# Kernel optimization log

Measured on AMD Instinct MI355X. Metric: run time of the kernel, lower is better.

The kernel has to match this reference:

```python
import jax, jax.numpy as jnp
import numpy as np

N = 100000      # nodes
E = 1600000     # edges (avg degree 16)
F_IN = 128
F_HID = 128
LN_EPS = 1e-5


def setup_inputs() -> dict:
    key = jax.random.key(0)
    ks = jax.random.split(key, 4)
    x = jax.random.normal(ks[0], (N, F_IN), dtype=jnp.float32)
    edge_index = jax.random.randint(ks[1], (2, E), 0, N, dtype=jnp.int32)
    W1 = jax.random.normal(ks[2], (F_IN, F_HID), dtype=jnp.float32) * 0.05
    W2 = jax.random.normal(ks[3], (F_HID, F_HID), dtype=jnp.float32) * 0.05
    return {
        "x": x,
        "edge_index": edge_index,
        "W1": W1, "b1": jnp.zeros((F_HID,), jnp.float32),
        "W2": W2, "b2": jnp.zeros((F_HID,), jnp.float32),
        "g1": jnp.ones((F_HID,), jnp.float32), "be1": jnp.zeros((F_HID,), jnp.float32),
        "g2": jnp.ones((F_HID,), jnp.float32), "be2": jnp.zeros((F_HID,), jnp.float32),
    }


def layer_norm(x, gamma, beta):
    mu = jnp.mean(x, axis=-1, keepdims=True)
    var = jnp.mean(jnp.square(x - mu), axis=-1, keepdims=True)
    return (x - mu) * jax.lax.rsqrt(var + LN_EPS) * gamma + beta


def gcn_conv(x, src, dst, W, b):
    """PyG GCNConv: linear transform, add self-loops, symmetric-normalized scatter-add."""
    n = x.shape[0]
    loop = jnp.arange(n, dtype=src.dtype)
    s = jnp.concatenate([src, loop])   # [E+N] sources (incl. self-loops)
    d = jnp.concatenate([dst, loop])   # [E+N] destinations
    deg = jax.ops.segment_sum(jnp.ones(s.shape[0], x.dtype), d, num_segments=n)
    dinv = jnp.where(deg > 0, jax.lax.rsqrt(deg), 0.0)
    norm = dinv[s] * dinv[d]           # [E+N] edge normalization
    h = x @ W                          # [N, F_hid] transform BEFORE propagate (PyG order)
    msg = h[s] * norm[:, None]         # [E+N, F_hid] gathered, normalized messages
    out = jax.ops.segment_sum(msg, d, num_segments=n)
    return out + b


def reference(x, edge_index, W1, b1, W2, b2, g1, be1, g2, be2):
    # GCN_body, layer=2, layer_norm_first=False, use_ln=True, eval mode (dropout=identity)
    src, dst = edge_index[0], edge_index[1]
    h = layer_norm(jax.nn.relu(gcn_conv(x, src, dst, W1, b1)), g1, be1)
    h = layer_norm(jax.nn.relu(gcn_conv(h, src, dst, W2, b2)), g2, be2)
    return h
```

## Files before the change

### kernel.cpp

```cpp
#include <hip/hip_runtime.h>

#define FDIM 128
#define LN_EPS 1e-5f
#define BSH 9
#define EPB 2048

typedef short short8 __attribute__((ext_vector_type(8)));
typedef float f32x4 __attribute__((ext_vector_type(4)));

__device__ __forceinline__ ushort f2bf(float f) {
    uint u = __float_as_uint(f);
    u += 0x7fff + ((u >> 16) & 1);
    return (ushort)(u >> 16);
}
__device__ __forceinline__ float bflo(uint u) { return __uint_as_float(u << 16); }
__device__ __forceinline__ float bfhi(uint u) { return __uint_as_float(u & 0xffff0000u); }


__global__ __launch_bounds__(256) void k_bcount(const int* __restrict__ dst,
                                                uint* __restrict__ mat, int nbk, int E) {
    __shared__ uint cnt[512];
    int t = threadIdx.x;
    for (int i = t; i < nbk; i += 256) cnt[i] = 0;
    __syncthreads();
    int base = blockIdx.x * EPB, end = min(base + EPB, E);
    for (int e = base + t; e < end; e += 256)
        atomicAdd(&cnt[(uint)dst[e] >> BSH], 1u);
    __syncthreads();
    for (int i = t; i < nbk; i += 256) mat[(size_t)blockIdx.x * nbk + i] = cnt[i];
}

__global__ __launch_bounds__(1024) void k_colscan(uint* __restrict__ mat,
                                                  uint* __restrict__ btot, int nbk, int nblk) {
    __shared__ uint s[1024];
    int b = blockIdx.x, t = threadIdx.x;
    uint run = 0;
    for (int base = 0; base < nblk; base += 1024) {
        int i = base + t;
        uint v = (i < nblk) ? mat[(size_t)i * nbk + b] : 0;
        s[t] = v;
        __syncthreads();
        for (int off = 1; off < 1024; off <<= 1) {
            uint u = (t >= off) ? s[t - off] : 0;
            __syncthreads();
            s[t] += u;
            __syncthreads();
        }
        if (i < nblk) mat[(size_t)i * nbk + b] = run + s[t] - v;
        run += s[1023];
        __syncthreads();
    }
    if (t == 0) btot[b] = run;
}

__global__ __launch_bounds__(256) void k_bscatter(const int* __restrict__ src,
                                                  const int* __restrict__ dst,
                                                  const uint* __restrict__ mat,
                                                  const uint* __restrict__ btot,
                                                  uint* __restrict__ ebuf, int nbk, int E) {
    __shared__ uint cur[512];
    __shared__ uint ps[256];
    int t = threadIdx.x;
    uint v = (t < nbk) ? btot[t] : 0;
    ps[t] = v;
    __syncthreads();
    for (int off = 1; off < 256; off <<= 1) {
        uint u = (t >= off) ? ps[t - off] : 0;
        __syncthreads();
        ps[t] += u;
        __syncthreads();
    }
    if (t < nbk) cur[t] = (ps[t] - v) + mat[(size_t)blockIdx.x * nbk + t];
    __syncthreads();
    int base = blockIdx.x * EPB, end = min(base + EPB, E);
    for (int e = base + t; e < end; e += 256) {
        uint d = (uint)dst[e];
        uint off = atomicAdd(&cur[d >> BSH], 1u);
        ebuf[off] = ((d & 511u) << 17) | (uint)src[e];
    }
}

__global__ __launch_bounds__(256) void k_bdeg(const uint* __restrict__ ebuf,
                                              const uint* __restrict__ btot,
                                              int* __restrict__ deg, float* __restrict__ dinv,
                                              uint* __restrict__ padtot, int N, int nbk) {
    __shared__ uint cnt[512];
    __shared__ uint ps[256];
    __shared__ uint begs;
    int b = blockIdx.x, t = threadIdx.x;
    for (int i = t; i < 512; i += 256) cnt[i] = 0;
    uint v = (t < nbk) ? btot[t] : 0;
    ps[t] = v;
    __syncthreads();
    for (int off = 1; off < 256; off <<= 1) {
        uint u = (t >= off) ? ps[t - off] : 0;
        __syncthreads();
        ps[t] += u;
        __syncthreads();
    }
    if (t == b) begs = ps[t] - v;
    __syncthreads();
    uint beg = begs, cn = btot[b];
    for (uint i = t; i < cn; i += 256) atomicAdd(&cnt[ebuf[beg + i] >> 17], 1u);
    __syncthreads();
    int n0 = b << BSH;
    uint loc = 0;
    for (int i = t; i < 512; i += 256) {
        int n = n0 + i;
        if (n < N) {
            uint dg = cnt[i];
            deg[n] = (int)dg;
            dinv[n] = rsqrtf((float)dg + 1.0f);
            loc += (dg + 7u) & ~7u;
        }
    }
    ps[t] = loc;
    __syncthreads();
    for (int off = 128; off >= 1; off >>= 1) {
        if (t < off) ps[t] += ps[t + off];
        __syncthreads();
    }
    if (t == 0) padtot[b] = ps[0];
}

__device__ __forceinline__ void bfill_body(const uint* __restrict__ ebuf,
                                           const uint* __restrict__ btot,
                                           const uint* __restrict__ padtot,
                                           const int* __restrict__ deg,
                                           int* __restrict__ rowptr, int* __restrict__ col,
                                           int N, int nbk, int b) {
    __shared__ uint ps[256];
    __shared__ uint lrp[512];
    __shared__ uint curf[512];
    __shared__ uint sc0, sc1;
    int t = threadIdx.x;
    uint v = (t < nbk) ? btot[t] : 0;
    ps[t] = v;
    __syncthreads();
    for (int off = 1; off < 256; off <<= 1) {
        uint u = (t >= off) ? ps[t - off] : 0;
        __syncthreads();
        ps[t] += u;
        __syncthreads();
    }
    if (t == b) sc0 = ps[t] - v;
    __syncthreads();
    uint w = (t < nbk) ? padtot[t] : 0;
    ps[t] = w;
    __syncthreads();
    for (int off = 1; off < 256; off <<= 1) {
        uint u = (t >= off) ? ps[t - off] : 0;
        __syncthreads();
        ps[t] += u;
        __syncthreads();
    }
    if (t == b) sc1 = ps[t] - w;
    if (b == nbk - 1 && t == nbk - 1) rowptr[N] = (int)ps[t];
    __syncthreads();
    uint beg = sc0, cn = btot[b], base = sc1;
    int n0 = b << BSH;
    int nA = n0 + 2 * t, nB = nA + 1;
    uint dA = (nA < N) ? (uint)deg[nA] : 0;
    uint dB = (nB < N) ? (uint)deg[nB] : 0;
    uint pA = (dA + 7u) & ~7u, pB = (dB + 7u) & ~7u;
    uint pair = pA + pB;
    ps[t] = pair;
    __syncthreads();
    for (int off = 1; off < 256; off <<= 1) {
        uint u = (t >= off) ? ps[t - off] : 0;
        __syncthreads();
        ps[t] += u;
        __syncthreads();
    }
    uint pex = ps[t] - pair;
    uint rA = base + pex, rB = rA + pA;
    lrp[2 * t] = rA; lrp[2 * t + 1] = rB;
    curf[2 * t] = rA; curf[2 * t + 1] = rB;
    if (nA < N) rowptr[nA] = (int)rA;
    if (nB < N) rowptr[nB] = (int)rB;
    if (nA < N) for (uint k = dA; k < pA; ++k) col[rA + k] = N;
    if (nB < N) for (uint k = dB; k < pB; ++k) col[rB + k] = N;
    __syncthreads();
    for (uint i = t; i < cn; i += 256) {
        uint e = ebuf[beg + i];
        uint p = atomicAdd(&curf[e >> 17], 1u);
        col[p] = (int)(e & 0x1FFFFu);
    }
}

__global__ void k_wt2(const float* __restrict__ W1, const float* __restrict__ W2,
                      ushort* __restrict__ WT1, ushort* __restrict__ WT2) {
    int b = blockIdx.x, k = threadIdx.x;
    if (b < 128) WT1[b * 128 + k] = f2bf(W1[k * 128 + b]);
    else         WT2[(b - 128) * 128 + k] = f2bf(W2[k * 128 + (b - 128)]);
}

template <bool F32IN>
__device__ __forceinline__ void gemm_body(char* sXb, char* sWb,
                                          const void* __restrict__ Xin,
                                          const ushort* __restrict__ WT,
                                          const float* __restrict__ dinv,
                                          ushort* __restrict__ H, int N, int bid) {
    int t = threadIdx.x;
    int w = t >> 6, lane = t & 63;
    int cl = lane & 15, kq = lane >> 4;
    int base = bid * 64;

    const short8* Wg = (const short8*)WT;
#pragma unroll
    for (int k = 0; k < 8; ++k) {
        int idx = t + k * 256;
        int c = idx >> 4, ch = idx & 15;
        *(short8*)(sWb + c * 256 + ((ch * 16) ^ ((c & 7) << 4))) = Wg[idx];
    }

    if constexpr (F32IN) {
        const float4* X4 = (const float4*)Xin;
        size_t lim = (size_t)N * 32 - 1;
#pragma unroll
        for (int k = 0; k < 8; ++k) {
            int idx = t + k * 256;
            size_t gi = (size_t)base * 32 + idx;
            float4 v = X4[gi < lim ? gi : lim];
            ushort4 o;
            o.x = f2bf(v.x); o.y = f2bf(v.y); o.z = f2bf(v.z); o.w = f2bf(v.w);
            int row = idx >> 5, b8 = (idx & 31) * 8;
            *(ushort4*)(sXb + row * 256 + (b8 ^ ((row & 7) << 4))) = o;
        }
    } else {
        const short8* X8 = (const short8*)Xin;
        size_t lim = (size_t)N * 16 - 1;
#pragma unroll
        for (int k = 0; k < 4; ++k) {
            int idx = t + k * 256;
            size_t gi = (size_t)base * 16 + idx;
            short8 v = X8[gi < lim ? gi : lim];
            int row = idx >> 4, b16 = (idx & 15) * 16;
            *(short8*)(sXb + row * 256 + (b16 ^ ((row & 7) << 4))) = v;
        }
    }
    __syncthreads();

    int rl = w * 16 + cl;
    short8 b0, b1, b2, b3;
#pragma unroll
    for (int kt = 0; kt < 4; ++kt) {
        short8 v = *(const short8*)(sXb + rl * 256 + ((kt * 64 + kq * 16) ^ ((rl & 7) << 4)));
        if (kt == 0) b0 = v; else if (kt == 1) b1 = v; else if (kt == 2) b2 = v; else b3 = v;
    }

    int r = base + rl;
    bool ok = r < N;
    float di = dinv[min(r, N - 1)];
#pragma unroll
    for (int nt = 0; nt < 8; ++nt) {
        int c = nt * 16 + cl;
        int sw = (c & 7) << 4;
        f32x4 acc = {0.f, 0.f, 0.f, 0.f};
        acc = __builtin_amdgcn_mfma_f32_16x16x32_bf16(
            *(const short8*)(sWb + c * 256 + ((0 * 64 + kq * 16) ^ sw)), b0, acc, 0, 0, 0);
        acc = __builtin_amdgcn_mfma_f32_16x16x32_bf16(
            *(const short8*)(sWb + c * 256 + ((1 * 64 + kq * 16) ^ sw)), b1, acc, 0, 0, 0);
        acc = __builtin_amdgcn_mfma_f32_16x16x32_bf16(
            *(const short8*)(sWb + c * 256 + ((2 * 64 + kq * 16) ^ sw)), b2, acc, 0, 0, 0);
        acc = __builtin_amdgcn_mfma_f32_16x16x32_bf16(
            *(const short8*)(sWb + c * 256 + ((3 * 64 + kq * 16) ^ sw)), b3, acc, 0, 0, 0);
        if (ok) {
            ushort4 o;
            o.x = f2bf(acc[0] * di); o.y = f2bf(acc[1] * di);
            o.z = f2bf(acc[2] * di); o.w = f2bf(acc[3] * di);
            *(ushort4*)(H + (size_t)r * 128 + nt * 16 + kq * 4) = o;
        }
    }
}

template <bool F32IN>
__global__ __launch_bounds__(256) void k_gemm(const void* __restrict__ Xin,
                                              const ushort* __restrict__ WT,
                                              const float* __restrict__ dinv,
                                              ushort* __restrict__ H, int N) {
    __shared__ ushort sX[64 * 128];
    __shared__ ushort sW[128 * 128];
    gemm_body<F32IN>((char*)sX, (char*)sW, Xin, WT, dinv, H, N, blockIdx.x);
}

__global__ __launch_bounds__(256) void k_mega(const void* __restrict__ Xin,
                                              const ushort* __restrict__ WT,
                                              const float* __restrict__ dinv,
                                              ushort* __restrict__ H, int N, int ngemm,
                                              const uint* __restrict__ ebuf,
                                              const uint* __restrict__ btot,
                                              const uint* __restrict__ padtot,
                                              const int* __restrict__ deg,
                                              int* __restrict__ rowptr,
                                              int* __restrict__ col, int nbk) {
    __shared__ ushort sX[64 * 128];
    __shared__ ushort sW[128 * 128];
    if (blockIdx.x < (uint)ngemm) {
        gemm_body<true>((char*)sX, (char*)sW, Xin, WT, dinv, H, N, blockIdx.x);
    } else {
        bfill_body(ebuf, btot, padtot, deg, rowptr, col, N, nbk, blockIdx.x - ngemm);
    }
}

__global__ __launch_bounds__(256) void k_agg(const uint4* __restrict__ H4,
                                             const int* __restrict__ rowptr,
                                             const int* __restrict__ col,
                                             const float* __restrict__ dinv,
                                             const float* __restrict__ bias,
                                             const float* __restrict__ gamma,
                                             const float* __restrict__ beta,
                                             float* __restrict__ outf,
                                             uint4* __restrict__ outb,
                                             int N) {
    int wave = threadIdx.x >> 6;
    int lane = threadIdx.x & 63;
    int q = lane >> 4;
    int l = lane & 15;
    int node = blockIdx.x * 16 + wave * 4 + q;
    bool valid = node < N;
    int nodec = valid ? node : N - 1;

    float di = dinv[nodec];
    uint4 hs = H4[(uint)nodec * 16u + (uint)l];
    float a0 = bflo(hs.x), a1 = bfhi(hs.x), a2 = bflo(hs.y), a3 = bfhi(hs.y);
    float a4 = bflo(hs.z), a5 = bfhi(hs.z), a6 = bflo(hs.w), a7 = bfhi(hs.w);

    int beg = rowptr[nodec];
    int deg8 = rowptr[nodec + 1] - beg;
    const int* cp = col + beg;

    for (int i = 0; i < deg8; i += 8) {
        int s0 = cp[i + 0], s1 = cp[i + 1], s2 = cp[i + 2], s3 = cp[i + 3];
        int s4 = cp[i + 4], s5 = cp[i + 5], s6 = cp[i + 6], s7 = cp[i + 7];
        uint4 u0 = H4[(uint)s0 * 16u + (uint)l];
        uint4 u1 = H4[(uint)s1 * 16u + (uint)l];
        uint4 u2 = H4[(uint)s2 * 16u + (uint)l];
        uint4 u3 = H4[(uint)s3 * 16u + (uint)l];
        uint4 u4 = H4[(uint)s4 * 16u + (uint)l];
        uint4 u5 = H4[(uint)s5 * 16u + (uint)l];
        uint4 u6 = H4[(uint)s6 * 16u + (uint)l];
        uint4 u7 = H4[(uint)s7 * 16u + (uint)l];
        a0 += bflo(u0.x); a1 += bfhi(u0.x); a2 += bflo(u0.y); a3 += bfhi(u0.y);
        a4 += bflo(u0.z); a5 += bfhi(u0.z); a6 += bflo(u0.w); a7 += bfhi(u0.w);
        a0 += bflo(u1.x); a1 += bfhi(u1.x); a2 += bflo(u1.y); a3 += bfhi(u1.y);
        a4 += bflo(u1.z); a5 += bfhi(u1.z); a6 += bflo(u1.w); a7 += bfhi(u1.w);
        a0 += bflo(u2.x); a1 += bfhi(u2.x); a2 += bflo(u2.y); a3 += bfhi(u2.y);
        a4 += bflo(u2.z); a5 += bfhi(u2.z); a6 += bflo(u2.w); a7 += bfhi(u2.w);
        a0 += bflo(u3.x); a1 += bfhi(u3.x); a2 += bflo(u3.y); a3 += bfhi(u3.y);
        a4 += bflo(u3.z); a5 += bfhi(u3.z); a6 += bflo(u3.w); a7 += bfhi(u3.w);
        a0 += bflo(u4.x); a1 += bfhi(u4.x); a2 += bflo(u4.y); a3 += bfhi(u4.y);
        a4 += bflo(u4.z); a5 += bfhi(u4.z); a6 += bflo(u4.w); a7 += bfhi(u4.w);
        a0 += bflo(u5.x); a1 += bfhi(u5.x); a2 += bflo(u5.y); a3 += bfhi(u5.y);
        a4 += bflo(u5.z); a5 += bfhi(u5.z); a6 += bflo(u5.w); a7 += bfhi(u5.w);
        a0 += bflo(u6.x); a1 += bfhi(u6.x); a2 += bflo(u6.y); a3 += bfhi(u6.y);
        a4 += bflo(u6.z); a5 += bfhi(u6.z); a6 += bflo(u6.w); a7 += bfhi(u6.w);
        a0 += bflo(u7.x); a1 += bfhi(u7.x); a2 += bflo(u7.y); a3 += bfhi(u7.y);
        a4 += bflo(u7.z); a5 += bfhi(u7.z); a6 += bflo(u7.w); a7 += bfhi(u7.w);
    }

    float4 bb0 = ((const float4*)bias)[2 * l];
    float4 bb1 = ((const float4*)bias)[2 * l + 1];
    a0 = fmaxf(fmaf(a0, di, bb0.x), 0.f);
    a1 = fmaxf(fmaf(a1, di, bb0.y), 0.f);
    a2 = fmaxf(fmaf(a2, di, bb0.z), 0.f);
    a3 = fmaxf(fmaf(a3, di, bb0.w), 0.f);
    a4 = fmaxf(fmaf(a4, di, bb1.x), 0.f);
    a5 = fmaxf(fmaf(a5, di, bb1.y), 0.f);
    a6 = fmaxf(fmaf(a6, di, bb1.z), 0.f);
    a7 = fmaxf(fmaf(a7, di, bb1.w), 0.f);

    float s1 = ((a0 + a1) + (a2 + a3)) + ((a4 + a5) + (a6 + a7));
    float s2 = ((a0 * a0 + a1 * a1) + (a2 * a2 + a3 * a3)) +
               ((a4 * a4 + a5 * a5) + (a6 * a6 + a7 * a7));
#pragma unroll
    for (int off = 8; off >= 1; off >>= 1) {
        s1 += __shfl_xor(s1, off);
        s2 += __shfl_xor(s2, off);
    }
    float mu = s1 * (1.f / 128.f);
    float var = s2 * (1.f / 128.f) - mu * mu;
    float rs = rsqrtf(var + LN_EPS);

    float4 g0 = ((const float4*)gamma)[2 * l];
    float4 g1 = ((const float4*)gamma)[2 * l + 1];
    float4 e0 = ((const float4*)beta)[2 * l];
    float4 e1 = ((const float4*)beta)[2 * l + 1];
    float o0 = (a0 - mu) * rs * g0.x + e0.x;
    float o1 = (a1 - mu) * rs * g0.y + e0.y;
    float o2 = (a2 - mu) * rs * g0.z + e0.z;
    float o3 = (a3 - mu) * rs * g0.w + e0.w;
    float o4 = (a4 - mu) * rs * g1.x + e1.x;
    float o5 = (a5 - mu) * rs * g1.y + e1.y;
    float o6 = (a6 - mu) * rs * g1.z + e1.z;
    float o7 = (a7 - mu) * rs * g1.w + e1.w;

    if (!valid) return;
    if (outf) {
        ((float4*)outf)[(size_t)node * 32 + 2 * l]     = make_float4(o0, o1, o2, o3);
        ((float4*)outf)[(size_t)node * 32 + 2 * l + 1] = make_float4(o4, o5, o6, o7);
    } else {
        uint4 o;
        o.x = (uint)f2bf(o0) | ((uint)f2bf(o1) << 16);
        o.y = (uint)f2bf(o2) | ((uint)f2bf(o3) << 16);
        o.z = (uint)f2bf(o4) | ((uint)f2bf(o5) << 16);
        o.w = (uint)f2bf(o6) | ((uint)f2bf(o7) << 16);
        outb[(size_t)node * 16 + l] = o;
    }
}

extern "C" void kernel_launch(void* const* d_in, const int* in_sizes, int n_in,
                              void* d_out, int out_size, void* d_ws, size_t ws_size,
                              hipStream_t stream) {
    const float* x  = (const float*)d_in[0];
    const int*   ei = (const int*)d_in[1];
    const float* W1 = (const float*)d_in[2];
    const float* b1 = (const float*)d_in[3];
    const float* W2 = (const float*)d_in[4];
    const float* b2 = (const float*)d_in[5];
    const float* g1 = (const float*)d_in[6];
    const float* be1 = (const float*)d_in[7];
    const float* g2 = (const float*)d_in[8];
    const float* be2 = (const float*)d_in[9];

    int N = in_sizes[0] / FDIM;
    int E = in_sizes[1] / 2;
    const int* srcp = ei;
    const int* dstp = ei + E;
    float* out = (float*)d_out;

    char* w = (char*)d_ws;
    size_t off = 0;
    auto take = [&](size_t bytes) {
        void* p = w + off;
        off = (off + bytes + 255) & ~(size_t)255;
        return p;
    };
    int nbk  = (N + 511) >> BSH;
    int nblk = (E + EPB - 1) / EPB;

    ushort* hb   = (ushort*)take((size_t)(N + 1) * FDIM * sizeof(ushort));
    ushort* WT1  = (ushort*)take(128 * 128 * sizeof(ushort));
    ushort* WT2  = (ushort*)take(128 * 128 * sizeof(ushort));
    uint* mat    = (uint*)take((size_t)nblk * nbk * sizeof(uint));
    uint* btot   = (uint*)take((size_t)nbk * sizeof(uint));
    uint* padtot = (uint*)take((size_t)nbk * sizeof(uint));
    uint* ebuf   = (uint*)take((size_t)E * sizeof(uint));
    int* deg     = (int*)take((size_t)N * sizeof(int));
    int* rowptr  = (int*)take((size_t)(N + 1) * sizeof(int));
    int* colb    = (int*)take((size_t)(E + 7 * (size_t)N + 1024) * sizeof(int));
    float* dinv  = (float*)take((size_t)N * sizeof(float));
    (void)ws_size;

    int ngemm = (N + 63) / 64;

    hipMemsetAsync(hb + (size_t)N * FDIM, 0, FDIM * sizeof(ushort), stream);

    k_wt2<<<256, 128, 0, stream>>>(W1, W2, WT1, WT2);

    k_bcount<<<nblk, 256, 0, stream>>>(dstp, mat, nbk, E);
    k_colscan<<<nbk, 1024, 0, stream>>>(mat, btot, nbk, nblk);
    k_bscatter<<<nblk, 256, 0, stream>>>(srcp, dstp, mat, btot, ebuf, nbk, E);
    k_bdeg<<<nbk, 256, 0, stream>>>(ebuf, btot, deg, dinv, padtot, N, nbk);

    k_mega<<<ngemm + nbk, 256, 0, stream>>>(x, WT1, dinv, hb, N, ngemm,
                                            ebuf, btot, padtot, deg, rowptr, colb, nbk);

    k_agg<<<(N + 15) / 16, 256, 0, stream>>>((const uint4*)hb, rowptr, colb, dinv,
                                             b1, g1, be1, nullptr, (uint4*)d_out, N);
    k_gemm<false><<<ngemm, 256, 0, stream>>>(d_out, WT2, dinv, hb, N);
    k_agg<<<(N + 15) / 16, 256, 0, stream>>>((const uint4*)hb, rowptr, colb, dinv,
                                             b2, g2, be2, out, nullptr, N);
}
```

Measured before the change: 221.7 us.

## Slice hidden features into eight column planes for cache-local aggregation

Stores the transformed features as eight 16-column slices so that each aggregation block gathers from a single 3.2MB slice. The goal is to keep the random neighbour gathers resident in cache. Because each block now sees only part of a row, LayerNorm is split into partial sums per slice, a small stats kernel, and a normalization step. That step is folded into the second GEMM's input load or done by a final apply kernel. It adds two extra kernels and extra traffic for the partial stats and the intermediate bf16 activations, and it reuses the output buffer and the edge-sort scratch as temporaries.

```diff
diff --git a/kernel.cpp b/kernel.cpp
--- a/kernel.cpp
+++ b/kernel.cpp
@@ -15,7 +15,7 @@
 }
 __device__ __forceinline__ float bflo(uint u) { return __uint_as_float(u << 16); }
 __device__ __forceinline__ float bfhi(uint u) { return __uint_as_float(u & 0xffff0000u); }
-
+__device__ __forceinline__ float bfs(short s) { return __uint_as_float(((uint)(ushort)s) << 16); }
 
 __global__ __launch_bounds__(256) void k_bcount(const int* __restrict__ dst,
                                                 uint* __restrict__ mat, int nbk, int E) {
@@ -130,7 +130,6 @@
                                            int* __restrict__ rowptr, int* __restrict__ col,
                                            int N, int nbk, int b) {
     __shared__ uint ps[256];
-    __shared__ uint lrp[512];
     __shared__ uint curf[512];
     __shared__ uint sc0, sc1;
     int t = threadIdx.x;
@@ -174,7 +173,6 @@
     }
     uint pex = ps[t] - pair;
     uint rA = base + pex, rB = rA + pA;
-    lrp[2 * t] = rA; lrp[2 * t + 1] = rB;
     curf[2 * t] = rA; curf[2 * t + 1] = rB;
     if (nA < N) rowptr[nA] = (int)rA;
     if (nB < N) rowptr[nB] = (int)rB;
@@ -189,17 +187,25 @@
 }
 
 __global__ void k_wt2(const float* __restrict__ W1, const float* __restrict__ W2,
-                      ushort* __restrict__ WT1, ushort* __restrict__ WT2) {
+                      ushort* __restrict__ WT1, ushort* __restrict__ WT2,
+                      ushort* __restrict__ H, int N) {
     int b = blockIdx.x, k = threadIdx.x;
-    if (b < 128) WT1[b * 128 + k] = f2bf(W1[k * 128 + b]);
-    else         WT2[(b - 128) * 128 + k] = f2bf(W2[k * 128 + (b - 128)]);
-}
-
-template <bool F32IN>
+    if (b < 128)      WT1[b * 128 + k] = f2bf(W1[k * 128 + b]);
+    else if (b < 256) WT2[(b - 128) * 128 + k] = f2bf(W2[k * 128 + (b - 128)]);
+    else if (k < 64) {
+        int s = k >> 3, j = k & 7;
+        ((uint*)(H + (size_t)s * (N + 1) * 16 + (size_t)N * 16))[j] = 0;
+    }
+}
+
+template <int MODE>
 __device__ __forceinline__ void gemm_body(char* sXb, char* sWb,
                                           const void* __restrict__ Xin,
                                           const ushort* __restrict__ WT,
                                           const float* __restrict__ dinv,
+                                          const float2* __restrict__ stats,
+                                          const float* __restrict__ gamma,
+                                          const float* __restrict__ beta,
                                           ushort* __restrict__ H, int N, int bid) {
     int t = threadIdx.x;
     int w = t >> 6, lane = t & 63;
@@ -214,7 +220,7 @@
         *(short8*)(sWb + c * 256 + ((ch * 16) ^ ((c & 7) << 4))) = Wg[idx];
     }
 
-    if constexpr (F32IN) {
+    if constexpr (MODE == 0) {
         const float4* X4 = (const float4*)Xin;
         size_t lim = (size_t)N * 32 - 1;
 #pragma unroll
@@ -228,15 +234,23 @@
             *(ushort4*)(sXb + row * 256 + (b8 ^ ((row & 7) << 4))) = o;
         }
     } else {
-        const short8* X8 = (const short8*)Xin;
-        size_t lim = (size_t)N * 16 - 1;
+        const short8* A8 = (const short8*)Xin;
+        size_t srows = (size_t)(N + 1) * 2;
 #pragma unroll
         for (int k = 0; k < 4; ++k) {
             int idx = t + k * 256;
-            size_t gi = (size_t)base * 16 + idx;
-            short8 v = X8[gi < lim ? gi : lim];
-            int row = idx >> 4, b16 = (idx & 15) * 16;
-            *(short8*)(sXb + row * 256 + (b16 ^ ((row & 7) << 4))) = v;
+            int row = idx >> 4, cc = idx & 15;
+            int rc = min(base + row, N - 1);
+            short8 v = A8[(size_t)(cc >> 1) * srows + (size_t)rc * 2 + (cc & 1)];
+            float2 ms = stats[rc];
+            short8 o;
+#pragma unroll
+            for (int j = 0; j < 8; ++j) {
+                int f = cc * 8 + j;
+                float val = (bfs(v[j]) - ms.x) * ms.y * gamma[f] + beta[f];
+                o[j] = (short)f2bf(val);
+            }
+            *(short8*)(sXb + row * 256 + ((cc * 16) ^ ((row & 7) << 4))) = o;
         }
     }
     __syncthreads();
@@ -269,19 +283,22 @@
             ushort4 o;
             o.x = f2bf(acc[0] * di); o.y = f2bf(acc[1] * di);
             o.z = f2bf(acc[2] * di); o.w = f2bf(acc[3] * di);
-            *(ushort4*)(H + (size_t)r * 128 + nt * 16 + kq * 4) = o;
-        }
-    }
-}
-
-template <bool F32IN>
+            *(ushort4*)(H + (size_t)nt * (N + 1) * 16 + (size_t)r * 16 + kq * 4) = o;
+        }
+    }
+}
+
+template <int MODE>
 __global__ __launch_bounds__(256) void k_gemm(const void* __restrict__ Xin,
                                               const ushort* __restrict__ WT,
                                               const float* __restrict__ dinv,
+                                              const float2* __restrict__ stats,
+                                              const float* __restrict__ gamma,
+                                              const float* __restrict__ beta,
                                               ushort* __restrict__ H, int N) {
     __shared__ ushort sX[64 * 128];
     __shared__ ushort sW[128 * 128];
-    gemm_body<F32IN>((char*)sX, (char*)sW, Xin, WT, dinv, H, N, blockIdx.x);
+    gemm_body<MODE>((char*)sX, (char*)sW, Xin, WT, dinv, stats, gamma, beta, H, N, blockIdx.x);
 }
 
 __global__ __launch_bounds__(256) void k_mega(const void* __restrict__ Xin,
@@ -297,116 +314,112 @@
     __shared__ ushort sX[64 * 128];
     __shared__ ushort sW[128 * 128];
     if (blockIdx.x < (uint)ngemm) {
-        gemm_body<true>((char*)sX, (char*)sW, Xin, WT, dinv, H, N, blockIdx.x);
+        gemm_body<0>((char*)sX, (char*)sW, Xin, WT, dinv, nullptr, nullptr, nullptr, H, N, blockIdx.x);
     } else {
         bfill_body(ebuf, btot, padtot, deg, rowptr, col, N, nbk, blockIdx.x - ngemm);
     }
 }
 
-__global__ __launch_bounds__(256) void k_agg(const uint4* __restrict__ H4,
-                                             const int* __restrict__ rowptr,
-                                             const int* __restrict__ col,
-                                             const float* __restrict__ dinv,
-                                             const float* __restrict__ bias,
-                                             const float* __restrict__ gamma,
-                                             const float* __restrict__ beta,
-                                             float* __restrict__ outf,
-                                             uint4* __restrict__ outb,
-                                             int N) {
-    int wave = threadIdx.x >> 6;
-    int lane = threadIdx.x & 63;
-    int q = lane >> 4;
-    int l = lane & 15;
-    int node = blockIdx.x * 16 + wave * 4 + q;
+__global__ __launch_bounds__(256) void k_agg_s(const ushort* __restrict__ Hs,
+                                               const int* __restrict__ rowptr,
+                                               const int* __restrict__ col,
+                                               const float* __restrict__ dinv,
+                                               const float* __restrict__ bias,
+                                               ushort* __restrict__ Aout,
+                                               float2* __restrict__ pstat, int N) {
+    int s = blockIdx.x & 7;
+    int chunk = blockIdx.x >> 3;
+    int w = threadIdx.x >> 6, lane = threadIdx.x & 63;
+    int g = lane >> 2, fl = lane & 3;
+    int node = chunk * 64 + w * 16 + g;
     bool valid = node < N;
     int nodec = valid ? node : N - 1;
 
+    const uint2* Hu = (const uint2*)(Hs + (size_t)s * (N + 1) * 16);
     float di = dinv[nodec];
-    uint4 hs = H4[(uint)nodec * 16u + (uint)l];
-    float a0 = bflo(hs.x), a1 = bfhi(hs.x), a2 = bflo(hs.y), a3 = bfhi(hs.y);
-    float a4 = bflo(hs.z), a5 = bfhi(hs.z), a6 = bflo(hs.w), a7 = bfhi(hs.w);
+    uint2 hv = Hu[(size_t)nodec * 4 + fl];
+    float a0 = bflo(hv.x), a1 = bfhi(hv.x), a2 = bflo(hv.y), a3 = bfhi(hv.y);
 
     int beg = rowptr[nodec];
     int deg8 = rowptr[nodec + 1] - beg;
     const int* cp = col + beg;
 
     for (int i = 0; i < deg8; i += 8) {
-        int s0 = cp[i + 0], s1 = cp[i + 1], s2 = cp[i + 2], s3 = cp[i + 3];
-        int s4 = cp[i + 4], s5 = cp[i + 5], s6 = cp[i + 6], s7 = cp[i + 7];
-        uint4 u0 = H4[(uint)s0 * 16u + (uint)l];
-        uint4 u1 = H4[(uint)s1 * 16u + (uint)l];
-        uint4 u2 = H4[(uint)s2 * 16u + (uint)l];
-        uint4 u3 = H4[(uint)s3 * 16u + (uint)l];
-        uint4 u4 = H4[(uint)s4 * 16u + (uint)l];
-        uint4 u5 = H4[(uint)s5 * 16u + (uint)l];
-        uint4 u6 = H4[(uint)s6 * 16u + (uint)l];
-        uint4 u7 = H4[(uint)s7 * 16u + (uint)l];
+        int e0 = cp[i + 0], e1 = cp[i + 1], e2 = cp[i + 2], e3 = cp[i + 3];
+        int e4 = cp[i + 4], e5 = cp[i + 5], e6 = cp[i + 6], e7 = cp[i + 7];
+        uint2 u0 = Hu[(size_t)e0 * 4 + fl];
+        uint2 u1 = Hu[(size_t)e1 * 4 + fl];
+        uint2 u2 = Hu[(size_t)e2 * 4 + fl];
+        uint2 u3 = Hu[(size_t)e3 * 4 + fl];
+        uint2 u4 = Hu[(size_t)e4 * 4 + fl];
+        uint2 u5 = Hu[(size_t)e5 * 4 + fl];
+        uint2 u6 = Hu[(size_t)e6 * 4 + fl];
+        uint2 u7 = Hu[(size_t)e7 * 4 + fl];
         a0 += bflo(u0.x); a1 += bfhi(u0.x); a2 += bflo(u0.y); a3 += bfhi(u0.y);
-        a4 += bflo(u0.z); a5 += bfhi(u0.z); a6 += bflo(u0.w); a7 += bfhi(u0.w);
         a0 += bflo(u1.x); a1 += bfhi(u1.x); a2 += bflo(u1.y); a3 += bfhi(u1.y);
-        a4 += bflo(u1.z); a5 += bfhi(u1.z); a6 += bflo(u1.w); a7 += bfhi(u1.w);
         a0 += bflo(u2.x); a1 += bfhi(u2.x); a2 += bflo(u2.y); a3 += bfhi(u2.y);
-        a4 += bflo(u2.z); a5 += bfhi(u2.z); a6 += bflo(u2.w); a7 += bfhi(u2.w);
         a0 += bflo(u3.x); a1 += bfhi(u3.x); a2 += bflo(u3.y); a3 += bfhi(u3.y);
-        a4 += bflo(u3.z); a5 += bfhi(u3.z); a6 += bflo(u3.w); a7 += bfhi(u3.w);
         a0 += bflo(u4.x); a1 += bfhi(u4.x); a2 += bflo(u4.y); a3 += bfhi(u4.y);
-        a4 += bflo(u4.z); a5 += bfhi(u4.z); a6 += bflo(u4.w); a7 += bfhi(u4.w);
         a0 += bflo(u5.x); a1 += bfhi(u5.x); a2 += bflo(u5.y); a3 += bfhi(u5.y);
-        a4 += bflo(u5.z); a5 += bfhi(u5.z); a6 += bflo(u5.w); a7 += bfhi(u5.w);
         a0 += bflo(u6.x); a1 += bfhi(u6.x); a2 += bflo(u6.y); a3 += bfhi(u6.y);
-        a4 += bflo(u6.z); a5 += bfhi(u6.z); a6 += bflo(u6.w); a7 += bfhi(u6.w);
         a0 += bflo(u7.x); a1 += bfhi(u7.x); a2 += bflo(u7.y); a3 += bfhi(u7.y);
-        a4 += bflo(u7.z); a5 += bfhi(u7.z); a6 += bflo(u7.w); a7 += bfhi(u7.w);
-    }
-
-    float4 bb0 = ((const float4*)bias)[2 * l];
-    float4 bb1 = ((const float4*)bias)[2 * l + 1];
-    a0 = fmaxf(fmaf(a0, di, bb0.x), 0.f);
-    a1 = fmaxf(fmaf(a1, di, bb0.y), 0.f);
-    a2 = fmaxf(fmaf(a2, di, bb0.z), 0.f);
-    a3 = fmaxf(fmaf(a3, di, bb0.w), 0.f);
-    a4 = fmaxf(fmaf(a4, di, bb1.x), 0.f);
-    a5 = fmaxf(fmaf(a5, di, bb1.y), 0.f);
-    a6 = fmaxf(fmaf(a6, di, bb1.z), 0.f);
-    a7 = fmaxf(fmaf(a7, di, bb1.w), 0.f);
-
-    float s1 = ((a0 + a1) + (a2 + a3)) + ((a4 + a5) + (a6 + a7));
-    float s2 = ((a0 * a0 + a1 * a1) + (a2 * a2 + a3 * a3)) +
-               ((a4 * a4 + a5 * a5) + (a6 * a6 + a7 * a7));
-#pragma unroll
-    for (int off = 8; off >= 1; off >>= 1) {
-        s1 += __shfl_xor(s1, off);
-        s2 += __shfl_xor(s2, off);
-    }
-    float mu = s1 * (1.f / 128.f);
-    float var = s2 * (1.f / 128.f) - mu * mu;
-    float rs = rsqrtf(var + LN_EPS);
-
-    float4 g0 = ((const float4*)gamma)[2 * l];
-    float4 g1 = ((const float4*)gamma)[2 * l + 1];
-    float4 e0 = ((const float4*)beta)[2 * l];
-    float4 e1 = ((const float4*)beta)[2 * l + 1];
-    float o0 = (a0 - mu) * rs * g0.x + e0.x;
-    float o1 = (a1 - mu) * rs * g0.y + e0.y;
-    float o2 = (a2 - mu) * rs * g0.z + e0.z;
-    float o3 = (a3 - mu) * rs * g0.w + e0.w;
-    float o4 = (a4 - mu) * rs * g1.x + e1.x;
-    float o5 = (a5 - mu) * rs * g1.y + e1.y;
-    float o6 = (a6 - mu) * rs * g1.z + e1.z;
-    float o7 = (a7 - mu) * rs * g1.w + e1.w;
+    }
+
+    float4 bb = ((const float4*)bias)[s * 4 + fl];
+    a0 = fmaxf(fmaf(a0, di, bb.x), 0.f);
+    a1 = fmaxf(fmaf(a1, di, bb.y), 0.f);
+    a2 = fmaxf(fmaf(a2, di, bb.z), 0.f);
+    a3 = fmaxf(fmaf(a3, di, bb.w), 0.f);
+
+    float s1 = (a0 + a1) + (a2 + a3);
+    float s2 = (a0 * a0 + a1 * a1) + (a2 * a2 + a3 * a3);
+    s1 += __shfl_xor(s1, 1); s1 += __shfl_xor(s1, 2);
+    s2 += __shfl_xor(s2, 1); s2 += __shfl_xor(s2, 2);
 
     if (!valid) return;
-    if (outf) {
-        ((float4*)outf)[(size_t)node * 32 + 2 * l]     = make_float4(o0, o1, o2, o3);
-        ((float4*)outf)[(size_t)node * 32 + 2 * l + 1] = make_float4(o4, o5, o6, o7);
-    } else {
-        uint4 o;
-        o.x = (uint)f2bf(o0) | ((uint)f2bf(o1) << 16);
-        o.y = (uint)f2bf(o2) | ((uint)f2bf(o3) << 16);
-        o.z = (uint)f2bf(o4) | ((uint)f2bf(o5) << 16);
-        o.w = (uint)f2bf(o6) | ((uint)f2bf(o7) << 16);
-        outb[(size_t)node * 16 + l] = o;
-    }
+    uint2 o;
+    o.x = (uint)f2bf(a0) | ((uint)f2bf(a1) << 16);
+    o.y = (uint)f2bf(a2) | ((uint)f2bf(a3) << 16);
+    ((uint2*)(Aout + (size_t)s * (N + 1) * 16))[(size_t)node * 4 + fl] = o;
+    if (fl == 0) pstat[(size_t)node * 8 + s] = make_float2(s1, s2);
+}
+
+__global__ void k_lnstat(const float2* __restrict__ pstat, float2* __restrict__ stats, int N) {
+    int i = blockIdx.x * 256 + threadIdx.x;
+    if (i < N) {
+        float s1 = 0.f, s2 = 0.f;
+#pragma unroll
+        for (int s = 0; s < 8; ++s) {
+            float2 p = pstat[(size_t)i * 8 + s];
+            s1 += p.x; s2 += p.y;
+        }
+        float mu = s1 * (1.f / 128.f);
+        float var = s2 * (1.f / 128.f) - mu * mu;
+        stats[i] = make_float2(mu, rsqrtf(var + LN_EPS));
+    }
+}
+
+__global__ void k_lnapply(const ushort* __restrict__ A, const float2* __restrict__ stats,
+                          const float* __restrict__ gamma, const float* __restrict__ beta,
+                          float* __restrict__ out, int N) {
+    int i = blockIdx.x * 256 + threadIdx.x;
+    if (i >= N * 16) return;
+    int node = i >> 4, cc = i & 15;
+    const short8* A8 = (const short8*)A;
+    size_t srows = (size_t)(N + 1) * 2;
+    short8 v = A8[(size_t)(cc >> 1) * srows + (size_t)node * 2 + (cc & 1)];
+    float2 ms = stats[node];
+    float4 o0, o1;
+    o0.x = (bfs(v[0]) - ms.x) * ms.y * gamma[cc * 8 + 0] + beta[cc * 8 + 0];
+    o0.y = (bfs(v[1]) - ms.x) * ms.y * gamma[cc * 8 + 1] + beta[cc * 8 + 1];
+    o0.z = (bfs(v[2]) - ms.x) * ms.y * gamma[cc * 8 + 2] + beta[cc * 8 + 2];
+    o0.w = (bfs(v[3]) - ms.x) * ms.y * gamma[cc * 8 + 3] + beta[cc * 8 + 3];
+    o1.x = (bfs(v[4]) - ms.x) * ms.y * gamma[cc * 8 + 4] + beta[cc * 8 + 4];
+    o1.y = (bfs(v[5]) - ms.x) * ms.y * gamma[cc * 8 + 5] + beta[cc * 8 + 5];
+    o1.z = (bfs(v[6]) - ms.x) * ms.y * gamma[cc * 8 + 6] + beta[cc * 8 + 6];
+    o1.w = (bfs(v[7]) - ms.x) * ms.y * gamma[cc * 8 + 7] + beta[cc * 8 + 7];
+    ((float4*)out)[(size_t)node * 32 + cc * 2]     = o0;
+    ((float4*)out)[(size_t)node * 32 + cc * 2 + 1] = o1;
 }
 
 extern "C" void kernel_launch(void* const* d_in, const int* in_sizes, int n_in,
@@ -439,36 +452,40 @@
     int nbk  = (N + 511) >> BSH;
     int nblk = (E + EPB - 1) / EPB;
 
-    ushort* hb   = (ushort*)take((size_t)(N + 1) * FDIM * sizeof(ushort));
-    ushort* WT1  = (ushort*)take(128 * 128 * sizeof(ushort));
-    ushort* WT2  = (ushort*)take(128 * 128 * sizeof(ushort));
-    uint* mat    = (uint*)take((size_t)nblk * nbk * sizeof(uint));
+    ushort* H   = (ushort*)take((size_t)(N + 1) * FDIM * sizeof(ushort));
+    ushort* A   = (ushort*)take((size_t)(N + 1) * FDIM * sizeof(ushort));
+    uint* ebuf  = (uint*)A;
+    uint* mat   = (uint*)((char*)A + (((size_t)E * 4 + 255) & ~(size_t)255));
+    ushort* WT1 = (ushort*)take(128 * 128 * sizeof(ushort));
+    ushort* WT2 = (ushort*)take(128 * 128 * sizeof(ushort));
     uint* btot   = (uint*)take((size_t)nbk * sizeof(uint));
     uint* padtot = (uint*)take((size_t)nbk * sizeof(uint));
-    uint* ebuf   = (uint*)take((size_t)E * sizeof(uint));
     int* deg     = (int*)take((size_t)N * sizeof(int));
     int* rowptr  = (int*)take((size_t)(N + 1) * sizeof(int));
     int* colb    = (int*)take((size_t)(E + 7 * (size_t)N + 1024) * sizeof(int));
     float* dinv  = (float*)take((size_t)N * sizeof(float));
+    float2* stats = (float2*)take((size_t)N * sizeof(float2));
+    float2* pstat = (float2*)d_out;
     (void)ws_size;
 
     int ngemm = (N + 63) / 64;
-
-    hipMemsetAsync(hb + (size_t)N * FDIM, 0, FDIM * sizeof(ushort), stream);
-
-    k_wt2<<<256, 128, 0, stream>>>(W1, W2, WT1, WT2);
+    int naggb = 8 * ((N + 63) / 64);
+
+    k_wt2<<<257, 128, 0, stream>>>(W1, W2, WT1, WT2, H, N);
 
     k_bcount<<<nblk, 256, 0, stream>>>(dstp, mat, nbk, E);
     k_colscan<<<nbk, 1024, 0, stream>>>(mat, btot, nbk, nblk);
     k_bscatter<<<nblk, 256, 0, stream>>>(srcp, dstp, mat, btot, ebuf, nbk, E);
     k_bdeg<<<nbk, 256, 0, stream>>>(ebuf, btot, deg, dinv, padtot, N, nbk);
 
-    k_mega<<<ngemm + nbk, 256, 0, stream>>>(x, WT1, dinv, hb, N, ngemm,
+    k_mega<<<ngemm + nbk, 256, 0, stream>>>(x, WT1, dinv, H, N, ngemm,
                                             ebuf, btot, padtot, deg, rowptr, colb, nbk);
 
-    k_agg<<<(N + 15) / 16, 256, 0, stream>>>((const uint4*)hb, rowptr, colb, dinv,
-                                             b1, g1, be1, nullptr, (uint4*)d_out, N);
-    k_gemm<false><<<ngemm, 256, 0, stream>>>(d_out, WT2, dinv, hb, N);
-    k_agg<<<(N + 15) / 16, 256, 0, stream>>>((const uint4*)hb, rowptr, colb, dinv,
-                                             b2, g2, be2, out, nullptr, N);
-}
+    k_agg_s<<<naggb, 256, 0, stream>>>(H, rowptr, colb, dinv, b1, A, pstat, N);
+    k_lnstat<<<(N + 255) / 256, 256, 0, stream>>>(pstat, stats, N);
+
+    k_gemm<1><<<ngemm, 256, 0, stream>>>(A, WT2, dinv, stats, g1, be1, H, N);
+    k_agg_s<<<naggb, 256, 0, stream>>>(H, rowptr, colb, dinv, b2, A, pstat, N);
+    k_lnstat<<<(N + 255) / 256, 256, 0, stream>>>(pstat, stats, N);
+    k_lnapply<<<(N * 16 + 255) / 256, 256, 0, stream>>>(A, stats, g2, be2, out, N);
+}
```

After: 285.1 us, median of 3. 28.6% more time.
